# Optimization experiments

Measured on AMD Instinct MI355X. Metric: run time of the kernel, lower is better.

Reference implementation:

```python
import jax, jax.numpy as jnp
import numpy as np

EMBED = 1024
HEADS = 16
HEAD_DIM = EMBED // HEADS
FFN_DIM = 4096
SEQ = 2048
BATCH = 2
EPS = 1e-5


def setup_inputs() -> dict:
    key = jax.random.key(0)
    ks = jax.random.split(key, 13)
    s = lambda n: 1.0 / np.sqrt(n)
    return {
        "x": jax.random.normal(ks[0], (BATCH, SEQ, EMBED), jnp.float32),
        # qkv projection (stored as [in, out])
        "w_qkv": jax.random.normal(ks[1], (EMBED, 3 * EMBED), jnp.float32) * s(EMBED),
        "b_qkv": jax.random.normal(ks[2], (3 * EMBED,), jnp.float32) * 0.02,
        "w_out": jax.random.normal(ks[3], (EMBED, EMBED), jnp.float32) * s(EMBED),
        "b_out": jax.random.normal(ks[4], (EMBED,), jnp.float32) * 0.02,
        # FFN
        "w_up": jax.random.normal(ks[5], (EMBED, FFN_DIM), jnp.float32) * s(EMBED),
        "b_up": jax.random.normal(ks[6], (FFN_DIM,), jnp.float32) * 0.02,
        "w_down": jax.random.normal(ks[7], (FFN_DIM, EMBED), jnp.float32) * s(FFN_DIM),
        "b_down": jax.random.normal(ks[8], (EMBED,), jnp.float32) * 0.02,
        # LayerNorms
        "g1": jnp.ones((EMBED,), jnp.float32),
        "be1": jnp.zeros((EMBED,), jnp.float32),
        "g2": jnp.ones((EMBED,), jnp.float32),
        "be2": jnp.zeros((EMBED,), jnp.float32),
    }


def _layernorm(x, g, b):
    mu = jnp.mean(x, axis=-1, keepdims=True)
    var = jnp.mean(jnp.square(x - mu), axis=-1, keepdims=True)
    return (x - mu) * jax.lax.rsqrt(var + EPS) * g + b


def reference(x, w_qkv, b_qkv, w_out, b_out, w_up, b_up, w_down, b_down, g1, be1, g2, be2):
    B, S, E = x.shape
    qkv = (x @ w_qkv + b_qkv).reshape(B, S, 3, HEADS, HEAD_DIM)
    qkv = jnp.transpose(qkv, (2, 0, 3, 1, 4))
    q, k, v = qkv[0], qkv[1], qkv[2]
    scale = 1.0 / jnp.sqrt(jnp.float32(HEAD_DIM))
    attn = jnp.einsum("bhqd,bhkd->bhqk", q, k) * scale  # [B,H,S,S]
    causal = jnp.tril(jnp.ones((S, S), bool))
    attn = jnp.where(causal, attn, -jnp.inf)
    attn = jax.nn.softmax(attn, axis=-1)
    out = jnp.einsum("bhqk,bhkd->bhqd", attn, v)  # [B,H,S,D]
    out = jnp.transpose(out, (0, 2, 1, 3)).reshape(B, S, E)
    attn_out = out @ w_out + b_out
    x = _layernorm(x + attn_out, g1, be1)
    ffn_out = jax.nn.relu(x @ w_up + b_up) @ w_down + b_down
    return _layernorm(x + ffn_out, g2, be2)
```

## Files before the change

kernel.cpp:

```cpp
#include <hip/hip_runtime.h>
#include <hip/hip_bf16.h>

#define EMBED 1024
#define HEADS 16
#define HDIM 64
#define FFN 4096
#define SEQ 2048
#define BATCH 2
#define MTOT (BATCH*SEQ)
#define QSCALE 0.1803368801111137f

typedef __attribute__((ext_vector_type(8))) short bf16x8;
typedef __attribute__((ext_vector_type(4))) float f32x4;
typedef __attribute__((ext_vector_type(16))) float f32x16;
typedef unsigned short u16;
typedef unsigned int u32;

__device__ __forceinline__ u16 f2bf(float f) {
  union { float f; unsigned u; } v; v.f = f;
  unsigned r = v.u + 0x7FFFu + ((v.u >> 16) & 1u);
  return (u16)(r >> 16);
}

__device__ __forceinline__ void async_ld16(const void* g, void* l) {
  __builtin_amdgcn_global_load_lds((const __attribute__((address_space(1))) void*)g,
                                   (__attribute__((address_space(3))) void*)l,
                                   16, 0, 0);
}

__device__ __forceinline__ void qkv_scatter(u16* qp, u16* kp, u16* vp,
                                            int row, int col, float v) {
  const int which = col >> 10, hh = (col >> 6) & 15, d = col & 63;
  const int bb = row >> 11, ss = row & 2047;
  const int bh = bb * 16 + hh;
  if (which == 0) {
    v *= QSCALE;
    size_t idx = ((((size_t)bh * 64 + (ss >> 5)) * 4 + (d >> 4)) << 9)
               + (((ss & 31) + 32 * ((d >> 3) & 1)) << 3) + (d & 7);
    qp[idx] = f2bf(v);
  } else if (which == 1) {
    size_t idx = ((((size_t)bh * 32 + (ss >> 6)) * 8 + (d >> 4) * 2 + ((ss >> 5) & 1)) << 9)
               + (((ss & 31) + 32 * ((d >> 3) & 1)) << 3) + (d & 7);
    kp[idx] = f2bf(v);
  } else {
    size_t idx = ((((size_t)bh * 32 + (ss >> 6)) * 8 + ((ss & 63) >> 4) * 2 + (d >> 5)) << 9)
               + (((d & 31) + 32 * ((ss >> 3) & 1)) << 3) + (ss & 7);
    vp[idx] = f2bf(v);
  }
}

__global__ __launch_bounds__(256) void k_cvt(const float* __restrict__ in,
                                             u16* __restrict__ out, int n4) {
  int i = blockIdx.x * 256 + threadIdx.x;
  int st = gridDim.x * 256;
  for (; i < n4; i += st) {
    float4 v = ((const float4*)in)[i];
    ushort4 o;
    o.x = f2bf(v.x); o.y = f2bf(v.y); o.z = f2bf(v.z); o.w = f2bf(v.w);
    ((ushort4*)out)[i] = o;
  }
}

__global__ __launch_bounds__(256) void k_tr(const float* __restrict__ w,
                                            u16* __restrict__ wT, int K, int N) {
  __shared__ u16 tile[32][33];
  int n0 = blockIdx.x * 32, k0 = blockIdx.y * 32;
  int tx = threadIdx.x, ty = threadIdx.y;
  #pragma unroll
  for (int i = 0; i < 4; ++i) {
    int k = k0 + ty + i * 8;
    tile[ty + i * 8][tx] = f2bf(w[(size_t)k * N + n0 + tx]);
  }
  __syncthreads();
  #pragma unroll
  for (int i = 0; i < 4; ++i) {
    int n = n0 + ty + i * 8;
    wT[(size_t)n * K + k0 + tx] = tile[tx][ty + i * 8];
  }
}

template <int OMODE, bool RELU>
__global__ __launch_bounds__(512) void k_gemm8(
    const u16* __restrict__ A, const u16* __restrict__ BT,
    const float* __restrict__ bias,
    void* __restrict__ out0, void* __restrict__ out1, void* __restrict__ out2,
    int M, int N, int K) {
  __shared__ __align__(16) u16 As[2][2][128 * 64];
  __shared__ __align__(16) u16 Bs[2][2][128 * 64];
  const int tid = threadIdx.x;
  const int lane = tid & 63, g = lane >> 4, li = lane & 15;
  const int wid = tid >> 6, wm = wid >> 2, wn = wid & 3;

  const int gx = gridDim.x;
  const int nwg = gx * gridDim.y;
  const int flat = blockIdx.y * gx + blockIdx.x;
  const int cpx = nwg >> 3;
  const int swz = (flat & 7) * cpx + (flat >> 3);
  const int m0 = (swz / gx) * 256, n0 = (swz % gx) * 256;

  f32x4 acc[8][4] = {};

  const u16* Ablk = A + (size_t)m0 * K;
  const u16* Bblk = BT + (size_t)n0 * K;
  const int trow = tid >> 3;
  const int sc = (tid & 7) ^ (trow & 7);

  auto stageA = [&](int buf, int h, int kt) {
    #pragma unroll
    for (int r = 0; r < 2; ++r)
      async_ld16(Ablk + (size_t)(h * 64 + r * 128 + trow) * K + kt + sc * 8,
                 &As[buf][h][0] + r * 4096 + tid * 8);
  };
  auto stageB = [&](int buf, int h, int kt) {
    #pragma unroll
    for (int r = 0; r < 2; ++r) {
      const int p = trow + r * 64;
      async_ld16(Bblk + (size_t)(((p >> 5) << 6) + h * 32 + (p & 31)) * K + kt + sc * 8,
                 &Bs[buf][h][0] + r * 4096 + tid * 8);
    }
  };

#define VM4_ asm volatile("s_waitcnt vmcnt(4)" ::: "memory")
#define VM2_ asm volatile("s_waitcnt vmcnt(2)" ::: "memory")
#define VM0_ asm volatile("s_waitcnt vmcnt(0)" ::: "memory")
#define VMN_
#define GP8(IH, JH, VMSTMT, STAGE_STMT) do {                                   \
    bf16x8 a_[4][2], b_[2][2];                                                 \
    _Pragma("unroll")                                                          \
    for (int i2 = 0; i2 < 4; ++i2) {                                           \
      const int pa = wm * 64 + i2 * 16 + li;                                   \
      _Pragma("unroll")                                                        \
      for (int ks = 0; ks < 2; ++ks)                                           \
        a_[i2][ks] = *(const bf16x8*)(&As[cur][IH][0] + pa * 64 +              \
                                      (((ks * 4 + g) ^ (li & 7)) * 8));        \
    }                                                                          \
    _Pragma("unroll")                                                          \
    for (int j2 = 0; j2 < 2; ++j2) {                                           \
      const int pb = wn * 32 + j2 * 16 + li;                                   \
      _Pragma("unroll")                                                        \
      for (int ks = 0; ks < 2; ++ks)                                           \
        b_[j2][ks] = *(const bf16x8*)(&Bs[cur][JH][0] + pb * 64 +              \
                                      (((ks * 4 + g) ^ (li & 7)) * 8));        \
    }                                                                          \
    STAGE_STMT;                                                                \
    VMSTMT;                                                                    \
    __builtin_amdgcn_s_barrier();                                              \
    asm volatile("s_waitcnt lgkmcnt(0)" ::: "memory");                         \
    __builtin_amdgcn_sched_barrier(0);                                         \
    __builtin_amdgcn_s_setprio(1);                                             \
    _Pragma("unroll")                                                          \
    for (int ks = 0; ks < 2; ++ks)                                             \
      _Pragma("unroll")                                                        \
      for (int i2 = 0; i2 < 4; ++i2)                                           \
        _Pragma("unroll")                                                      \
        for (int j2 = 0; j2 < 2; ++j2)                                         \
          acc[IH * 4 + i2][JH * 2 + j2] = __builtin_amdgcn_mfma_f32_16x16x32_bf16( \
              a_[i2][ks], b_[j2][ks], acc[IH * 4 + i2][JH * 2 + j2], 0, 0, 0); \
    __builtin_amdgcn_s_setprio(0);                                             \
    __builtin_amdgcn_s_barrier();                                              \
    asm volatile("" ::: "memory");                                             \
  } while (0)

  stageA(0, 0, 0); stageB(0, 0, 0); stageA(0, 1, 0); stageB(0, 1, 0);
  VM4_;
  __builtin_amdgcn_s_barrier();
  asm volatile("" ::: "memory");

  int cur = 0;
  const int nkt = K >> 6;
  for (int t = 0; t < nkt - 1; ++t) {
    const int kn = (t + 1) * 64;
    GP8(0, 0, VM4_, stageA(cur ^ 1, 0, kn));
    GP8(1, 0, VM4_, stageB(cur ^ 1, 0, kn));
    GP8(0, 1, VMN_, stageA(cur ^ 1, 1, kn));
    GP8(1, 1, VM4_, stageB(cur ^ 1, 1, kn));
    cur ^= 1;
  }
  GP8(0, 0, VM2_, );
  GP8(1, 0, VM0_, );
  GP8(0, 1, VMN_, );
  GP8(1, 1, VMN_, );
#undef GP8
#undef VM4_
#undef VM2_
#undef VM0_
#undef VMN_

  float bcol[4];
  #pragma unroll
  for (int j = 0; j < 4; ++j) bcol[j] = bias[n0 + wn * 64 + j * 16 + li];

  #pragma unroll
  for (int i = 0; i < 8; ++i) {
    #pragma unroll
    for (int j = 0; j < 4; ++j) {
      #pragma unroll
      for (int r = 0; r < 4; ++r) {
        int row = m0 + wm * 128 + i * 16 + g * 4 + r;
        int col = n0 + wn * 64 + j * 16 + li;
        float v = acc[i][j][r] + bcol[j];
        if (RELU) v = fmaxf(v, 0.f);
        if (OMODE == 0) {
          ((u16*)out0)[(size_t)row * N + col] = f2bf(v);
        } else {
          qkv_scatter((u16*)out0, (u16*)out1, (u16*)out2, row, col, v);
        }
      }
    }
  }
}

template <int BN, int BK, int OMODE, bool RELU>
__global__ __launch_bounds__(256) void k_gemm(
    const u16* __restrict__ A, const u16* __restrict__ BT,
    const float* __restrict__ bias,
    void* __restrict__ out0, void* __restrict__ out1, void* __restrict__ out2,
    int M, int N, int K) {
  constexpr int NR = BN / 32;
  constexpr int KS = BK / 32;
  constexpr int TPR = BK / 8;
  constexpr int RPI = 256 / TPR;
  constexpr int CM = TPR - 1;

  __shared__ u16 As[2][128 * BK];
  __shared__ u16 Bs[2][BN * BK];
  const int tid = threadIdx.x;
  const int lane = tid & 63, g = lane >> 4, li = lane & 15;
  const int wid = tid >> 6, wm = wid >> 1, wn = wid & 1;

  const int gx = gridDim.x;
  const int nwg = gx * gridDim.y;
  const int flat = blockIdx.y * gx + blockIdx.x;
  const int cpx = nwg >> 3;
  const int swz = (flat & 7) * cpx + (flat >> 3);
  const int m0 = (swz / gx) * 128, n0 = (swz % gx) * BN;

  f32x4 acc[4][NR] = {};

  const u16* Ablk = A + (size_t)m0 * K;
  const u16* Bblk = BT + (size_t)n0 * K;
  const int srow = tid / TPR;
  const int scol = ((tid % TPR) ^ (srow & CM)) * 8;

  auto stage = [&](int buf, int kt) {
    #pragma unroll
    for (int r = 0; r < 128; r += RPI)
      async_ld16(Ablk + (size_t)(srow + r) * K + kt + scol, &As[buf][(srow + r) * BK] + (tid % TPR) * 8);
    #pragma unroll
    for (int r = 0; r < BN; r += RPI)
      async_ld16(Bblk + (size_t)(srow + r) * K + kt + scol, &Bs[buf][(srow + r) * BK] + (tid % TPR) * 8);
  };

  stage(0, 0);
  int cur = 0;
  for (int kt = 0; kt < K; kt += BK) {
    __syncthreads();
    if (kt + BK < K) stage(cur ^ 1, kt + BK);

    bf16x8 af[4][KS], bfr[NR][KS];
    #pragma unroll
    for (int i = 0; i < 4; ++i) {
      const int row = wm * 64 + i * 16 + li;
      #pragma unroll
      for (int ks = 0; ks < KS; ++ks) {
        const int c = ks * 4 + g;
        af[i][ks] = *(const bf16x8*)(&As[cur][row * BK] + ((c ^ (row & CM)) & CM) * 8);
      }
    }
    #pragma unroll
    for (int j = 0; j < NR; ++j) {
      const int row = wn * (BN / 2) + j * 16 + li;
      #pragma unroll
      for (int ks = 0; ks < KS; ++ks) {
        const int c = ks * 4 + g;
        bfr[j][ks] = *(const bf16x8*)(&Bs[cur][row * BK] + ((c ^ (row & CM)) & CM) * 8);
      }
    }
    #pragma unroll
    for (int ks = 0; ks < KS; ++ks)
      #pragma unroll
      for (int i = 0; i < 4; ++i)
        #pragma unroll
        for (int j = 0; j < NR; ++j)
          acc[i][j] = __builtin_amdgcn_mfma_f32_16x16x32_bf16(af[i][ks], bfr[j][ks], acc[i][j], 0, 0, 0);
    cur ^= 1;
  }

  float bcol[NR];
  #pragma unroll
  for (int j = 0; j < NR; ++j) bcol[j] = bias[n0 + wn * (BN / 2) + j * 16 + li];

  #pragma unroll
  for (int i = 0; i < 4; ++i) {
    #pragma unroll
    for (int j = 0; j < NR; ++j) {
      #pragma unroll
      for (int r = 0; r < 4; ++r) {
        int row = m0 + wm * 64 + i * 16 + g * 4 + r;
        int col = n0 + wn * (BN / 2) + j * 16 + li;
        float v = acc[i][j][r] + bcol[j];
        if (RELU) v = fmaxf(v, 0.f);
        if (OMODE == 0) {
          ((u16*)out0)[(size_t)row * N + col] = f2bf(v);
        } else if (OMODE == 1) {
          ((float*)out0)[(size_t)row * N + col] = v;
        } else {
          qkv_scatter((u16*)out0, (u16*)out1, (u16*)out2, row, col, v);
        }
      }
    }
  }
}

__global__ __launch_bounds__(256, 3) void k_attn7(
    const u16* __restrict__ Qp, const u16* __restrict__ Kp,
    const u16* __restrict__ Vp, u16* __restrict__ ctx) {
  const int bh = blockIdx.x;
  const int t32 = 63 - (int)blockIdx.y;
  const int b = bh >> 4, h = bh & 15;
  const int tid = threadIdx.x;
  const int wid = tid >> 6, lane = tid & 63;
  const int ql = lane & 31, hl = lane >> 5;

  __shared__ __align__(16) float mrg[3][64][34];

  const int wq0 = t32 * 32;
  const int qg = wq0 + ql;
  const int nt = ((wq0 + 31) >> 6) + 1;

  bf16x8 qf[4];
  {
    const u16* qpb = Qp + ((((size_t)bh * 64 + t32) * 4) << 9) + lane * 8;
    #pragma unroll
    for (int d4 = 0; d4 < 4; ++d4)
      qf[d4] = *(const bf16x8*)(qpb + (d4 << 9));
  }

  const u16* kbase = Kp + (((size_t)bh * 32) << 12) + lane * 8;
  const u16* vbase = Vp + (((size_t)bh * 32) << 12) + lane * 8;

  f32x16 o0 = {}, o1 = {};
  float m_run = -1e30f, l_run = 0.f;

  for (int kt = wid; kt < nt; kt += 4) {
    const bool kh1 = (kt * 64 + 32 <= wq0 + 31);
    const bool domask = (kt * 64 + (kh1 ? 63 : 31) > wq0);
    const u16* kb_ = kbase + ((size_t)kt << 12);
    const u16* vb_ = vbase + ((size_t)kt << 12);

    bf16x8 kf0[4], kf1[4];
    #pragma unroll
    for (int d4 = 0; d4 < 4; ++d4) {
      kf0[d4] = *(const bf16x8*)(kb_ + ((d4 * 2 + 0) << 9));
      if (kh1) kf1[d4] = *(const bf16x8*)(kb_ + ((d4 * 2 + 1) << 9));
    }
    bf16x8 vf0[4], vf1[4];
    #pragma unroll
    for (int t = 0; t < 4; ++t)
      if (t < 2 || kh1) {
        vf0[t] = *(const bf16x8*)(vb_ + ((t * 2 + 0) << 9));
        vf1[t] = *(const bf16x8*)(vb_ + ((t * 2 + 1) << 9));
      }

    f32x16 S0 = {}, S1 = {};
    #pragma unroll
    for (int d4 = 0; d4 < 4; ++d4)
      S0 = __builtin_amdgcn_mfma_f32_32x32x16_bf16(kf0[d4], qf[d4], S0, 0, 0, 0);
    if (kh1) {
      #pragma unroll
      for (int d4 = 0; d4 < 4; ++d4)
        S1 = __builtin_amdgcn_mfma_f32_32x32x16_bf16(kf1[d4], qf[d4], S1, 0, 0, 0);
    }

    if (domask) {
      const int qrel = qg - kt * 64 - 4 * hl;
      #pragma unroll
      for (int r = 0; r < 16; ++r) {
        const int kc = (r & 3) + 8 * (r >> 2);
        S0[r] = (kc <= qrel) ? S0[r] : -3.0e38f;
      }
      if (kh1) {
        #pragma unroll
        for (int r = 0; r < 16; ++r) {
          const int kc = 32 + (r & 3) + 8 * (r >> 2);
          S1[r] = (kc <= qrel) ? S1[r] : -3.0e38f;
        }
      }
    }

    float mt = -3.0e38f;
    #pragma unroll
    for (int r = 0; r < 16; ++r) mt = fmaxf(mt, S0[r]);
    if (kh1) {
      #pragma unroll
      for (int r = 0; r < 16; ++r) mt = fmaxf(mt, S1[r]);
    }
    mt = fmaxf(mt, __shfl_xor(mt, 32, 64));

    if (!__all(mt <= m_run + 8.0f)) {
      const float mn = fmaxf(m_run, mt);
      const float alpha = exp2f(m_run - mn);
      l_run *= alpha;
      o0 *= alpha;
      o1 *= alpha;
      m_run = mn;
    }
    float sum = 0.f;
    #pragma unroll
    for (int r = 0; r < 16; ++r) { S0[r] = exp2f(S0[r] - m_run); sum += S0[r]; }
    if (kh1) {
      #pragma unroll
      for (int r = 0; r < 16; ++r) { S1[r] = exp2f(S1[r] - m_run); sum += S1[r]; }
    }
    sum += __shfl_xor(sum, 32, 64);
    l_run += sum;

    u32 pk[2][8], sw[2][8];
    #pragma unroll
    for (int m = 0; m < 4; ++m) {
      asm("v_cvt_pk_bf16_f32 %0, %1, %2" : "=v"(pk[0][2*m])   : "v"(S0[4*m+0]), "v"(S0[4*m+1]));
      asm("v_cvt_pk_bf16_f32 %0, %1, %2" : "=v"(pk[0][2*m+1]) : "v"(S0[4*m+2]), "v"(S0[4*m+3]));
    }
    #pragma unroll
    for (int i = 0; i < 8; ++i) sw[0][i] = __shfl_xor(pk[0][i], 32, 64);
    if (kh1) {
      #pragma unroll
      for (int m = 0; m < 4; ++m) {
        asm("v_cvt_pk_bf16_f32 %0, %1, %2" : "=v"(pk[1][2*m])   : "v"(S1[4*m+0]), "v"(S1[4*m+1]));
        asm("v_cvt_pk_bf16_f32 %0, %1, %2" : "=v"(pk[1][2*m+1]) : "v"(S1[4*m+2]), "v"(S1[4*m+3]));
      }
      #pragma unroll
      for (int i = 0; i < 8; ++i) sw[1][i] = __shfl_xor(pk[1][i], 32, 64);
    }

    #pragma unroll
    for (int t = 0; t < 4; ++t) {
      if (t < 2 || kh1) {
        const int c = t >> 1, m0 = 2 * (t & 1), m1 = m0 + 1;
        union { u32 u[4]; bf16x8 v; } pf;
        pf.u[0] = hl ? sw[c][2*m1]   : pk[c][2*m0];
        pf.u[1] = hl ? sw[c][2*m1+1] : pk[c][2*m0+1];
        pf.u[2] = hl ? pk[c][2*m1]   : sw[c][2*m0];
        pf.u[3] = hl ? pk[c][2*m1+1] : sw[c][2*m0+1];
        o0 = __builtin_amdgcn_mfma_f32_32x32x16_bf16(vf0[t], pf.v, o0, 0, 0, 0);
        o1 = __builtin_amdgcn_mfma_f32_32x32x16_bf16(vf1[t], pf.v, o1, 0, 0, 0);
      }
    }
  }

  if (wid > 0) {
    float* p = &mrg[wid - 1][lane][0];
    *(f32x16*)(p) = o0;
    *(f32x16*)(p + 16) = o1;
    p[32] = m_run;
    p[33] = l_run;
  }
  __syncthreads();
  if (wid > 0) return;

  float M = m_run;
  #pragma unroll
  for (int w = 0; w < 3; ++w) M = fmaxf(M, mrg[w][lane][32]);
  const float fa = exp2f(m_run - M);
  f32x16 acc0 = o0 * fa, acc1 = o1 * fa;
  float L = l_run * fa;
  #pragma unroll
  for (int w = 0; w < 3; ++w) {
    const float* p = &mrg[w][lane][0];
    const float fw = exp2f(p[32] - M);
    L += p[33] * fw;
    f32x16 t0 = *(const f32x16*)(p);
    f32x16 t1 = *(const f32x16*)(p + 16);
    acc0 += t0 * fw;
    acc1 += t1 * fw;
  }
  const float inv = 1.f / L;

  u16* outp = ctx + (size_t)(b * SEQ + qg) * EMBED + h * HDIM + 4 * hl;
  #pragma unroll
  for (int m = 0; m < 4; ++m) {
    ushort4 s0v, s1v;
    s0v.x = f2bf(acc0[4*m+0] * inv); s0v.y = f2bf(acc0[4*m+1] * inv);
    s0v.z = f2bf(acc0[4*m+2] * inv); s0v.w = f2bf(acc0[4*m+3] * inv);
    *(ushort4*)(outp + 8 * m) = s0v;
    s1v.x = f2bf(acc1[4*m+0] * inv); s1v.y = f2bf(acc1[4*m+1] * inv);
    s1v.z = f2bf(acc1[4*m+2] * inv); s1v.w = f2bf(acc1[4*m+3] * inv);
    *(ushort4*)(outp + 32 + 8 * m) = s1v;
  }
}

__global__ __launch_bounds__(256) void k_add_ln(
    const float* __restrict__ a, const float* __restrict__ bmat,
    const float* __restrict__ gam, const float* __restrict__ bet,
    float* __restrict__ outf, u16* __restrict__ outb) {
  const int row = blockIdx.x;
  const int t = threadIdx.x;
  __shared__ float red[8];
  float4 va = ((const float4*)(a + (size_t)row * EMBED))[t];
  float4 vb = ((const float4*)(bmat + (size_t)row * EMBED))[t];
  float s0 = va.x + vb.x, s1 = va.y + vb.y, s2 = va.z + vb.z, s3 = va.w + vb.w;
  float sum = s0 + s1 + s2 + s3;
  float sq = s0 * s0 + s1 * s1 + s2 * s2 + s3 * s3;
  #pragma unroll
  for (int m = 1; m < 64; m <<= 1) {
    sum += __shfl_xor(sum, m, 64);
    sq += __shfl_xor(sq, m, 64);
  }
  int wid = t >> 6;
  if ((t & 63) == 0) { red[wid] = sum; red[4 + wid] = sq; }
  __syncthreads();
  sum = red[0] + red[1] + red[2] + red[3];
  sq = red[4] + red[5] + red[6] + red[7];
  float mean = sum * (1.f / EMBED);
  float var = sq * (1.f / EMBED) - mean * mean;
  float rstd = rsqrtf(var + 1e-5f);
  float4 gv = ((const float4*)gam)[t], bev = ((const float4*)bet)[t];
  float y0 = (s0 - mean) * rstd * gv.x + bev.x;
  float y1 = (s1 - mean) * rstd * gv.y + bev.y;
  float y2 = (s2 - mean) * rstd * gv.z + bev.z;
  float y3 = (s3 - mean) * rstd * gv.w + bev.w;
  float4 o; o.x = y0; o.y = y1; o.z = y2; o.w = y3;
  ((float4*)(outf + (size_t)row * EMBED))[t] = o;
  if (outb) {
    ushort4 ob; ob.x = f2bf(y0); ob.y = f2bf(y1); ob.z = f2bf(y2); ob.w = f2bf(y3);
    ((ushort4*)(outb + (size_t)row * EMBED))[t] = ob;
  }
}

extern "C" void kernel_launch(void* const* d_in, const int* in_sizes, int n_in,
                              void* d_out, int out_size, void* d_ws, size_t ws_size,
                              hipStream_t stream) {
  const float* x      = (const float*)d_in[0];
  const float* w_qkv  = (const float*)d_in[1];
  const float* b_qkv  = (const float*)d_in[2];
  const float* w_out  = (const float*)d_in[3];
  const float* b_out  = (const float*)d_in[4];
  const float* w_up   = (const float*)d_in[5];
  const float* b_up   = (const float*)d_in[6];
  const float* w_down = (const float*)d_in[7];
  const float* b_down = (const float*)d_in[8];
  const float* g1  = (const float*)d_in[9];
  const float* be1 = (const float*)d_in[10];
  const float* g2  = (const float*)d_in[11];
  const float* be2 = (const float*)d_in[12];

  char* ws = (char*)d_ws;
  size_t off = 0;
  auto alloc = [&](size_t bytes) { void* p = ws + off; off += (bytes + 255) & ~(size_t)255; return p; };

  u16* xb     = (u16*)alloc((size_t)MTOT * EMBED * 2);
  u16* wqkvT  = (u16*)alloc((size_t)3 * EMBED * EMBED * 2);
  u16* woutT  = (u16*)alloc((size_t)EMBED * EMBED * 2);
  u16* wupT   = (u16*)alloc((size_t)FFN * EMBED * 2);
  u16* wdownT = (u16*)alloc((size_t)EMBED * FFN * 2);
  u16* qp     = (u16*)alloc((size_t)MTOT * EMBED * 2);
  u16* kp     = (u16*)alloc((size_t)MTOT * EMBED * 2);
  u16* vp     = (u16*)alloc((size_t)MTOT * EMBED * 2);
  u16* ctx    = (u16*)alloc((size_t)MTOT * EMBED * 2);
  float* attn_proj = (float*)alloc((size_t)MTOT * EMBED * 4);
  float* y_f32     = (float*)alloc((size_t)MTOT * EMBED * 4);
  u16* y_bf16      = (u16*)alloc((size_t)MTOT * EMBED * 2);
  u16* hmid        = (u16*)alloc((size_t)MTOT * FFN * 2);
  float* ffn_o     = (float*)alloc((size_t)MTOT * EMBED * 4);

  dim3 trb(32, 8);
  k_cvt<<<2048, 256, 0, stream>>>(x, xb, MTOT * EMBED / 4);
  k_tr<<<dim3(3 * EMBED / 32, EMBED / 32), trb, 0, stream>>>(w_qkv, wqkvT, EMBED, 3 * EMBED);
  k_tr<<<dim3(EMBED / 32, EMBED / 32), trb, 0, stream>>>(w_out, woutT, EMBED, EMBED);
  k_tr<<<dim3(FFN / 32, EMBED / 32), trb, 0, stream>>>(w_up, wupT, EMBED, FFN);
  k_tr<<<dim3(EMBED / 32, FFN / 32), trb, 0, stream>>>(w_down, wdownT, FFN, EMBED);

  k_gemm8<2, false><<<dim3(3 * EMBED / 256, MTOT / 256), 512, 0, stream>>>(
      xb, wqkvT, b_qkv, qp, kp, vp, MTOT, 3 * EMBED, EMBED);

  k_attn7<<<dim3(BATCH * HEADS, 64), 256, 0, stream>>>(qp, kp, vp, ctx);

  k_gemm<64, 64, 1, false><<<dim3(EMBED / 64, MTOT / 128), 256, 0, stream>>>(
      ctx, woutT, b_out, attn_proj, nullptr, nullptr, MTOT, EMBED, EMBED);

  k_add_ln<<<MTOT, 256, 0, stream>>>(x, attn_proj, g1, be1, y_f32, y_bf16);

  k_gemm8<0, true><<<dim3(FFN / 256, MTOT / 256), 512, 0, stream>>>(
      y_bf16, wupT, b_up, hmid, nullptr, nullptr, MTOT, FFN, EMBED);

  k_gemm<64, 64, 1, false><<<dim3(EMBED / 64, MTOT / 128), 256, 0, stream>>>(
      hmid, wdownT, b_down, ffn_o, nullptr, nullptr, MTOT, EMBED, FFN);

  k_add_ln<<<MTOT, 256, 0, stream>>>(y_f32, ffn_o, g2, be2, (float*)d_out, nullptr);

  (void)in_sizes; (void)n_in; (void)out_size; (void)ws_size;
}
```

Measured before the change: 241.4 us.

## Split-K the out-projection and down-projection GEMMs, reduce partials in LayerNorm

The two narrow-N GEMMs (out-proj and FFN down-proj) now run with a 2-way split-K grid dimension, each half writing fp32 partials to a separate buffer. The bias add and the partial sum move into a new add+LayerNorm kernel that reads both partials. This doubles the workgroup count for GEMMs that launch only 512 blocks, to fill the GPU better. The cost is extra fp32 partial-buffer traffic, written by the GEMMs and read back in the LayerNorm kernel.

```diff
diff --git a/kernel.cpp b/kernel.cpp
--- a/kernel.cpp
+++ b/kernel.cpp
@@ -210,12 +210,12 @@
   }
 }
 
-template <int BN, int BK, int OMODE, bool RELU>
+template <int BN, int BK, bool RELU>
 __global__ __launch_bounds__(256) void k_gemm(
     const u16* __restrict__ A, const u16* __restrict__ BT,
     const float* __restrict__ bias,
-    void* __restrict__ out0, void* __restrict__ out1, void* __restrict__ out2,
-    int M, int N, int K) {
+    void* __restrict__ out0, void* __restrict__ out1,
+    int M, int N, int K, int ldk) {
   constexpr int NR = BN / 32;
   constexpr int KS = BK / 32;
   constexpr int TPR = BK / 8;
@@ -227,6 +227,10 @@
   const int tid = threadIdx.x;
   const int lane = tid & 63, g = lane >> 4, li = lane & 15;
   const int wid = tid >> 6, wm = wid >> 1, wn = wid & 1;
+  const int kc = blockIdx.z;
+
+  A += (size_t)kc * K;
+  BT += (size_t)kc * K;
 
   const int gx = gridDim.x;
   const int nwg = gx * gridDim.y;
@@ -237,18 +241,18 @@
 
   f32x4 acc[4][NR] = {};
 
-  const u16* Ablk = A + (size_t)m0 * K;
-  const u16* Bblk = BT + (size_t)n0 * K;
+  const u16* Ablk = A + (size_t)m0 * ldk;
+  const u16* Bblk = BT + (size_t)n0 * ldk;
   const int srow = tid / TPR;
   const int scol = ((tid % TPR) ^ (srow & CM)) * 8;
 
   auto stage = [&](int buf, int kt) {
     #pragma unroll
     for (int r = 0; r < 128; r += RPI)
-      async_ld16(Ablk + (size_t)(srow + r) * K + kt + scol, &As[buf][(srow + r) * BK] + (tid % TPR) * 8);
+      async_ld16(Ablk + (size_t)(srow + r) * ldk + kt + scol, &As[buf][(srow + r) * BK] + (tid % TPR) * 8);
     #pragma unroll
     for (int r = 0; r < BN; r += RPI)
-      async_ld16(Bblk + (size_t)(srow + r) * K + kt + scol, &Bs[buf][(srow + r) * BK] + (tid % TPR) * 8);
+      async_ld16(Bblk + (size_t)(srow + r) * ldk + kt + scol, &Bs[buf][(srow + r) * BK] + (tid % TPR) * 8);
   };
 
   stage(0, 0);
@@ -288,8 +292,9 @@
 
   float bcol[NR];
   #pragma unroll
-  for (int j = 0; j < NR; ++j) bcol[j] = bias[n0 + wn * (BN / 2) + j * 16 + li];
-
+  for (int j = 0; j < NR; ++j) bcol[j] = bias ? bias[n0 + wn * (BN / 2) + j * 16 + li] : 0.f;
+
+  float* outp = (float*)(kc == 0 ? out0 : out1);
   #pragma unroll
   for (int i = 0; i < 4; ++i) {
     #pragma unroll
@@ -300,13 +305,7 @@
         int col = n0 + wn * (BN / 2) + j * 16 + li;
         float v = acc[i][j][r] + bcol[j];
         if (RELU) v = fmaxf(v, 0.f);
-        if (OMODE == 0) {
-          ((u16*)out0)[(size_t)row * N + col] = f2bf(v);
-        } else if (OMODE == 1) {
-          ((float*)out0)[(size_t)row * N + col] = v;
-        } else {
-          qkv_scatter((u16*)out0, (u16*)out1, (u16*)out2, row, col, v);
-        }
+        outp[(size_t)row * N + col] = v;
       }
     }
   }
@@ -489,16 +488,22 @@
   }
 }
 
-__global__ __launch_bounds__(256) void k_add_ln(
-    const float* __restrict__ a, const float* __restrict__ bmat,
+__global__ __launch_bounds__(256) void k_add_ln3(
+    const float* __restrict__ a, const float* __restrict__ p0,
+    const float* __restrict__ p1, const float* __restrict__ bias,
     const float* __restrict__ gam, const float* __restrict__ bet,
     float* __restrict__ outf, u16* __restrict__ outb) {
   const int row = blockIdx.x;
   const int t = threadIdx.x;
   __shared__ float red[8];
   float4 va = ((const float4*)(a + (size_t)row * EMBED))[t];
-  float4 vb = ((const float4*)(bmat + (size_t)row * EMBED))[t];
-  float s0 = va.x + vb.x, s1 = va.y + vb.y, s2 = va.z + vb.z, s3 = va.w + vb.w;
+  float4 v0 = ((const float4*)(p0 + (size_t)row * EMBED))[t];
+  float4 v1 = ((const float4*)(p1 + (size_t)row * EMBED))[t];
+  float4 bv = ((const float4*)bias)[t];
+  float s0 = va.x + v0.x + v1.x + bv.x;
+  float s1 = va.y + v0.y + v1.y + bv.y;
+  float s2 = va.z + v0.z + v1.z + bv.z;
+  float s3 = va.w + v0.w + v1.w + bv.w;
   float sum = s0 + s1 + s2 + s3;
   float sq = s0 * s0 + s1 * s1 + s2 * s2 + s3 * s3;
   #pragma unroll
@@ -519,8 +524,10 @@
   float y1 = (s1 - mean) * rstd * gv.y + bev.y;
   float y2 = (s2 - mean) * rstd * gv.z + bev.z;
   float y3 = (s3 - mean) * rstd * gv.w + bev.w;
-  float4 o; o.x = y0; o.y = y1; o.z = y2; o.w = y3;
-  ((float4*)(outf + (size_t)row * EMBED))[t] = o;
+  if (outf) {
+    float4 o; o.x = y0; o.y = y1; o.z = y2; o.w = y3;
+    ((float4*)(outf + (size_t)row * EMBED))[t] = o;
+  }
   if (outb) {
     ushort4 ob; ob.x = f2bf(y0); ob.y = f2bf(y1); ob.z = f2bf(y2); ob.w = f2bf(y3);
     ((ushort4*)(outb + (size_t)row * EMBED))[t] = ob;
@@ -557,11 +564,13 @@
   u16* kp     = (u16*)alloc((size_t)MTOT * EMBED * 2);
   u16* vp     = (u16*)alloc((size_t)MTOT * EMBED * 2);
   u16* ctx    = (u16*)alloc((size_t)MTOT * EMBED * 2);
-  float* attn_proj = (float*)alloc((size_t)MTOT * EMBED * 4);
-  float* y_f32     = (float*)alloc((size_t)MTOT * EMBED * 4);
-  u16* y_bf16      = (u16*)alloc((size_t)MTOT * EMBED * 2);
-  u16* hmid        = (u16*)alloc((size_t)MTOT * FFN * 2);
-  float* ffn_o     = (float*)alloc((size_t)MTOT * EMBED * 4);
+  float* ap0  = (float*)alloc((size_t)MTOT * EMBED * 4);
+  float* ap1  = (float*)alloc((size_t)MTOT * EMBED * 4);
+  float* y_f32 = (float*)alloc((size_t)MTOT * EMBED * 4);
+  u16* y_bf16  = (u16*)alloc((size_t)MTOT * EMBED * 2);
+  u16* hmid    = (u16*)alloc((size_t)MTOT * FFN * 2);
+  float* fp0   = (float*)alloc((size_t)MTOT * EMBED * 4);
+  float* fp1   = (float*)alloc((size_t)MTOT * EMBED * 4);
 
   dim3 trb(32, 8);
   k_cvt<<<2048, 256, 0, stream>>>(x, xb, MTOT * EMBED / 4);
@@ -575,18 +584,18 @@
 
   k_attn7<<<dim3(BATCH * HEADS, 64), 256, 0, stream>>>(qp, kp, vp, ctx);
 
-  k_gemm<64, 64, 1, false><<<dim3(EMBED / 64, MTOT / 128), 256, 0, stream>>>(
-      ctx, woutT, b_out, attn_proj, nullptr, nullptr, MTOT, EMBED, EMBED);
-
-  k_add_ln<<<MTOT, 256, 0, stream>>>(x, attn_proj, g1, be1, y_f32, y_bf16);
+  k_gemm<64, 64, false><<<dim3(EMBED / 64, MTOT / 128, 2), 256, 0, stream>>>(
+      ctx, woutT, nullptr, ap0, ap1, MTOT, EMBED, EMBED / 2, EMBED);
+
+  k_add_ln3<<<MTOT, 256, 0, stream>>>(x, ap0, ap1, b_out, g1, be1, y_f32, y_bf16);
 
   k_gemm8<0, true><<<dim3(FFN / 256, MTOT / 256), 512, 0, stream>>>(
       y_bf16, wupT, b_up, hmid, nullptr, nullptr, MTOT, FFN, EMBED);
 
-  k_gemm<64, 64, 1, false><<<dim3(EMBED / 64, MTOT / 128), 256, 0, stream>>>(
-      hmid, wdownT, b_down, ffn_o, nullptr, nullptr, MTOT, EMBED, FFN);
-
-  k_add_ln<<<MTOT, 256, 0, stream>>>(y_f32, ffn_o, g2, be2, (float*)d_out, nullptr);
+  k_gemm<64, 64, false><<<dim3(EMBED / 64, MTOT / 128, 2), 256, 0, stream>>>(
+      hmid, wdownT, nullptr, fp0, fp1, MTOT, EMBED, FFN / 2, FFN);
+
+  k_add_ln3<<<MTOT, 256, 0, stream>>>(y_f32, fp0, fp1, b_down, g2, be2, (float*)d_out, nullptr);
 
   (void)in_sizes; (void)n_in; (void)out_size; (void)ws_size;
 }
```

Result: slower. 253.1 us (+4.9%).

## Rewrite out-proj and down-proj GEMM with 4-stage async pipeline and 128x128 tiles

Applied to the files above, without the earlier changes.

Replaces the double-buffered 128x64 GEMM used for the output and FFN down projections with a 128x128 tile kernel. It uses a 4-deep LDS ring with BK=32 and explicit vmcnt waits, raw s_barrier and setprio around the MFMA block. The aim is to hide global-load latency and to increase per-block data reuse for the two N=1024 GEMMs. The trade-off is half as many workgroups (256 blocks), which lowers occupancy, plus hand-managed wait counts that must stay correct. It also adds an unused null check on the fp32 output in the layernorm.

```diff
diff --git a/kernel.cpp b/kernel.cpp
--- a/kernel.cpp
+++ b/kernel.cpp
@@ -210,20 +210,13 @@
   }
 }
 
-template <int BN, int BK, int OMODE, bool RELU>
-__global__ __launch_bounds__(256) void k_gemm(
+template <bool RELU>
+__global__ __launch_bounds__(256) void k_gemm3(
     const u16* __restrict__ A, const u16* __restrict__ BT,
-    const float* __restrict__ bias,
-    void* __restrict__ out0, void* __restrict__ out1, void* __restrict__ out2,
+    const float* __restrict__ bias, float* __restrict__ out,
     int M, int N, int K) {
-  constexpr int NR = BN / 32;
-  constexpr int KS = BK / 32;
-  constexpr int TPR = BK / 8;
-  constexpr int RPI = 256 / TPR;
-  constexpr int CM = TPR - 1;
-
-  __shared__ u16 As[2][128 * BK];
-  __shared__ u16 Bs[2][BN * BK];
+  __shared__ __align__(16) u16 As[4][128 * 32];
+  __shared__ __align__(16) u16 Bs[4][128 * 32];
   const int tid = threadIdx.x;
   const int lane = tid & 63, g = lane >> 4, li = lane & 15;
   const int wid = tid >> 6, wm = wid >> 1, wn = wid & 1;
@@ -233,80 +226,84 @@
   const int flat = blockIdx.y * gx + blockIdx.x;
   const int cpx = nwg >> 3;
   const int swz = (flat & 7) * cpx + (flat >> 3);
-  const int m0 = (swz / gx) * 128, n0 = (swz % gx) * BN;
-
-  f32x4 acc[4][NR] = {};
+  const int m0 = (swz / gx) * 128, n0 = (swz % gx) * 128;
+
+  f32x4 acc[4][4] = {};
 
   const u16* Ablk = A + (size_t)m0 * K;
   const u16* Bblk = BT + (size_t)n0 * K;
-  const int srow = tid / TPR;
-  const int scol = ((tid % TPR) ^ (srow & CM)) * 8;
+  const int trow = tid >> 2;
+  const int sc = ((tid & 3) ^ (trow & 3)) * 8;
 
   auto stage = [&](int buf, int kt) {
     #pragma unroll
-    for (int r = 0; r < 128; r += RPI)
-      async_ld16(Ablk + (size_t)(srow + r) * K + kt + scol, &As[buf][(srow + r) * BK] + (tid % TPR) * 8);
-    #pragma unroll
-    for (int r = 0; r < BN; r += RPI)
-      async_ld16(Bblk + (size_t)(srow + r) * K + kt + scol, &Bs[buf][(srow + r) * BK] + (tid % TPR) * 8);
+    for (int r = 0; r < 2; ++r) {
+      async_ld16(Ablk + (size_t)(trow + r * 64) * K + kt + sc,
+                 &As[buf][0] + r * 2048 + tid * 8);
+      async_ld16(Bblk + (size_t)(trow + r * 64) * K + kt + sc,
+                 &Bs[buf][0] + r * 2048 + tid * 8);
+    }
   };
 
-  stage(0, 0);
+#define GM_VM8 asm volatile("s_waitcnt vmcnt(8)" ::: "memory")
+#define GM_VM4 asm volatile("s_waitcnt vmcnt(4)" ::: "memory")
+#define GM_VM0 asm volatile("s_waitcnt vmcnt(0)" ::: "memory")
+
+  stage(0, 0); stage(1, 32); stage(2, 64);
+  GM_VM8;
+  __builtin_amdgcn_s_barrier();
+  asm volatile("" ::: "memory");
+
   int cur = 0;
-  for (int kt = 0; kt < K; kt += BK) {
-    __syncthreads();
-    if (kt + BK < K) stage(cur ^ 1, kt + BK);
-
-    bf16x8 af[4][KS], bfr[NR][KS];
+  for (int kt = 0; kt < K; kt += 32) {
+    bf16x8 af[4], bfr[4];
     #pragma unroll
     for (int i = 0; i < 4; ++i) {
       const int row = wm * 64 + i * 16 + li;
-      #pragma unroll
-      for (int ks = 0; ks < KS; ++ks) {
-        const int c = ks * 4 + g;
-        af[i][ks] = *(const bf16x8*)(&As[cur][row * BK] + ((c ^ (row & CM)) & CM) * 8);
-      }
-    }
-    #pragma unroll
-    for (int j = 0; j < NR; ++j) {
-      const int row = wn * (BN / 2) + j * 16 + li;
-      #pragma unroll
-      for (int ks = 0; ks < KS; ++ks) {
-        const int c = ks * 4 + g;
-        bfr[j][ks] = *(const bf16x8*)(&Bs[cur][row * BK] + ((c ^ (row & CM)) & CM) * 8);
-      }
-    }
-    #pragma unroll
-    for (int ks = 0; ks < KS; ++ks)
-      #pragma unroll
-      for (int i = 0; i < 4; ++i)
-        #pragma unroll
-        for (int j = 0; j < NR; ++j)
-          acc[i][j] = __builtin_amdgcn_mfma_f32_16x16x32_bf16(af[i][ks], bfr[j][ks], acc[i][j], 0, 0, 0);
-    cur ^= 1;
-  }
-
-  float bcol[NR];
-  #pragma unroll
-  for (int j = 0; j < NR; ++j) bcol[j] = bias[n0 + wn * (BN / 2) + j * 16 + li];
+      af[i] = *(const bf16x8*)(&As[cur][0] + row * 32 + ((g ^ (row & 3)) * 8));
+    }
+    #pragma unroll
+    for (int j = 0; j < 4; ++j) {
+      const int row = wn * 64 + j * 16 + li;
+      bfr[j] = *(const bf16x8*)(&Bs[cur][0] + row * 32 + ((g ^ (row & 3)) * 8));
+    }
+    if (kt + 96 < K) stage((cur + 3) & 3, kt + 96);
+    if (kt + 96 < K)      GM_VM8;
+    else if (kt + 64 < K) GM_VM4;
+    else if (kt + 32 < K) GM_VM0;
+    __builtin_amdgcn_s_barrier();
+    asm volatile("s_waitcnt lgkmcnt(0)" ::: "memory");
+    __builtin_amdgcn_sched_barrier(0);
+    __builtin_amdgcn_s_setprio(1);
+    #pragma unroll
+    for (int i = 0; i < 4; ++i)
+      #pragma unroll
+      for (int j = 0; j < 4; ++j)
+        acc[i][j] = __builtin_amdgcn_mfma_f32_16x16x32_bf16(af[i], bfr[j], acc[i][j], 0, 0, 0);
+    __builtin_amdgcn_s_setprio(0);
+    __builtin_amdgcn_s_barrier();
+    asm volatile("" ::: "memory");
+    cur = (cur + 1) & 3;
+  }
+#undef GM_VM8
+#undef GM_VM4
+#undef GM_VM0
+
+  float bcol[4];
+  #pragma unroll
+  for (int j = 0; j < 4; ++j) bcol[j] = bias[n0 + wn * 64 + j * 16 + li];
 
   #pragma unroll
   for (int i = 0; i < 4; ++i) {
     #pragma unroll
-    for (int j = 0; j < NR; ++j) {
+    for (int j = 0; j < 4; ++j) {
       #pragma unroll
       for (int r = 0; r < 4; ++r) {
         int row = m0 + wm * 64 + i * 16 + g * 4 + r;
-        int col = n0 + wn * (BN / 2) + j * 16 + li;
+        int col = n0 + wn * 64 + j * 16 + li;
         float v = acc[i][j][r] + bcol[j];
         if (RELU) v = fmaxf(v, 0.f);
-        if (OMODE == 0) {
-          ((u16*)out0)[(size_t)row * N + col] = f2bf(v);
-        } else if (OMODE == 1) {
-          ((float*)out0)[(size_t)row * N + col] = v;
-        } else {
-          qkv_scatter((u16*)out0, (u16*)out1, (u16*)out2, row, col, v);
-        }
+        out[(size_t)row * N + col] = v;
       }
     }
   }
@@ -519,8 +516,10 @@
   float y1 = (s1 - mean) * rstd * gv.y + bev.y;
   float y2 = (s2 - mean) * rstd * gv.z + bev.z;
   float y3 = (s3 - mean) * rstd * gv.w + bev.w;
-  float4 o; o.x = y0; o.y = y1; o.z = y2; o.w = y3;
-  ((float4*)(outf + (size_t)row * EMBED))[t] = o;
+  if (outf) {
+    float4 o; o.x = y0; o.y = y1; o.z = y2; o.w = y3;
+    ((float4*)(outf + (size_t)row * EMBED))[t] = o;
+  }
   if (outb) {
     ushort4 ob; ob.x = f2bf(y0); ob.y = f2bf(y1); ob.z = f2bf(y2); ob.w = f2bf(y3);
     ((ushort4*)(outb + (size_t)row * EMBED))[t] = ob;
@@ -575,16 +574,16 @@
 
   k_attn7<<<dim3(BATCH * HEADS, 64), 256, 0, stream>>>(qp, kp, vp, ctx);
 
-  k_gemm<64, 64, 1, false><<<dim3(EMBED / 64, MTOT / 128), 256, 0, stream>>>(
-      ctx, woutT, b_out, attn_proj, nullptr, nullptr, MTOT, EMBED, EMBED);
+  k_gemm3<false><<<dim3(EMBED / 128, MTOT / 128), 256, 0, stream>>>(
+      ctx, woutT, b_out, attn_proj, MTOT, EMBED, EMBED);
 
   k_add_ln<<<MTOT, 256, 0, stream>>>(x, attn_proj, g1, be1, y_f32, y_bf16);
 
   k_gemm8<0, true><<<dim3(FFN / 256, MTOT / 256), 512, 0, stream>>>(
       y_bf16, wupT, b_up, hmid, nullptr, nullptr, MTOT, FFN, EMBED);
 
-  k_gemm<64, 64, 1, false><<<dim3(EMBED / 64, MTOT / 128), 256, 0, stream>>>(
-      hmid, wdownT, b_down, ffn_o, nullptr, nullptr, MTOT, EMBED, FFN);
+  k_gemm3<false><<<dim3(EMBED / 128, MTOT / 128), 256, 0, stream>>>(
+      hmid, wdownT, b_down, ffn_o, MTOT, EMBED, FFN);
 
   k_add_ln<<<MTOT, 256, 0, stream>>>(y_f32, ffn_o, g2, be2, (float*)d_out, nullptr);
 
```

Result: no change. 242.5 us (+0.5%).
